# Kernel optimization log

Measured on AMD Instinct MI355X. Metric: run time of the kernel, lower is better.

Reference implementation:

```python
import jax, jax.numpy as jnp
import numpy as np
from jax.ops import segment_sum, segment_max

N = 100000          # nodes
E = 1600000         # edges
F_NODE = 128
F_EDGE = 32
HID = 64
ACT = 32
NG = 1000           # graph rows in y (repeat_factor = N // NG = 100)
NEG_SLOPE = 0.2


def _add_self_loops(src, dst, ea, n):
    # PyG add_self_loops with fill_value='mean': self-loop attr = mean of
    # incoming edge_attr per target node (0 for isolated nodes).
    cnt = segment_sum(jnp.ones((ea.shape[0],), ea.dtype), dst, num_segments=n)
    loop_attr = segment_sum(ea, dst, num_segments=n) / jnp.clip(cnt, 1.0)[:, None]
    ar = jnp.arange(n, dtype=src.dtype)
    return (jnp.concatenate([src, ar]),
            jnp.concatenate([dst, ar]),
            jnp.concatenate([ea, loop_attr], axis=0))


def _gatv2(xx, src, dst, ea, Wl, bl, Wr, br, We, att, bias, n):
    xl = xx @ Wl + bl                      # source transform  [n, HID]
    xr = xx @ Wr + br                      # target transform  [n, HID]
    e = ea @ We                            # edge embedding    [E', HID]
    m = jax.nn.leaky_relu(xl[src] + xr[dst] + e, NEG_SLOPE)
    logits = m @ att                       # [E']
    mx = segment_max(logits, dst, num_segments=n)
    ex = jnp.exp(logits - mx[dst])
    den = segment_sum(ex, dst, num_segments=n)
    alpha = ex / den[dst]                  # segment softmax over incoming edges
    return segment_sum(xl[src] * alpha[:, None], dst, num_segments=n) + bias


def setup_inputs() -> dict:
    key = jax.random.key(0)
    ks = jax.random.split(key, 32)
    g = lambda k, s: jax.random.normal(k, s, jnp.float32)
    p = lambda k, s: jax.random.normal(k, s, jnp.float32) * 0.05
    return {
        "x": g(ks[0], (N, F_NODE)),
        "edge_attr": g(ks[1], (E, F_EDGE)),
        "y": g(ks[2], (2 * NG,)),
        "Wl1": p(ks[3], (F_NODE, HID)), "bl1": p(ks[4], (HID,)),
        "Wr1": p(ks[5], (F_NODE, HID)), "br1": p(ks[6], (HID,)),
        "We1": p(ks[7], (F_EDGE, HID)), "att1": p(ks[8], (HID,)),
        "bias1": p(ks[9], (HID,)),
        "Wl2": p(ks[10], (HID, HID)), "bl2": p(ks[11], (HID,)),
        "Wr2": p(ks[12], (HID, HID)), "br2": p(ks[13], (HID,)),
        "We2": p(ks[14], (F_EDGE, HID)), "att2": p(ks[15], (HID,)),
        "bias2": p(ks[16], (HID,)),
        "W0": p(ks[17], (2, 2)), "b0": p(ks[18], (2,)),
        "W1": p(ks[19], (HID + 2, 32)), "b1": p(ks[20], (32,)),
        "W2": p(ks[21], (32, ACT)), "b2": p(ks[22], (ACT,)),
        "edge_index": jax.random.randint(ks[23], (2, E), 0, N),
        "node_idx": jax.random.randint(ks[24], (1000,), 0, N),
    }


def reference(x, edge_attr, y, Wl1, bl1, Wr1, br1, We1, att1, bias1,
              Wl2, bl2, Wr2, br2, We2, att2, bias2,
              W0, b0, W1, b1, W2, b2, edge_index, node_idx):
    n = x.shape[0]
    src, dst, ea = _add_self_loops(edge_index[0], edge_index[1], edge_attr, n)
    h = jax.nn.relu(_gatv2(x, src, dst, ea, Wl1, bl1, Wr1, br1, We1, att1, bias1, n))
    h = jax.nn.relu(_gatv2(h, src, dst, ea, Wl2, bl2, Wr2, br2, We2, att2, bias2, n))
    yr = y.reshape(-1, 2)
    repeat_factor = n // yr.shape[0]
    yr = jnp.repeat(yr, repeat_factor, axis=0)          # [n, 2]
    yr = jax.nn.relu(yr @ W0 + b0)
    z = jnp.concatenate([h, yr], axis=1)                # [n, HID+2]
    z = jax.nn.relu(z @ W1 + b1)
    z = z @ W2 + b2                                     # [n, ACT]
    return z[node_idx]
```

## Files before the change

kernel.cpp:

```cpp
#include <hip/hip_runtime.h>


#define NF1CAP 24576

__device__ __forceinline__ int getbit(const unsigned* b, int i) {
    return (b[i >> 5] >> (i & 31)) & 1;
}

__global__ __launch_bounds__(256)
void mark_sel_kernel(const int* __restrict__ nidx, unsigned* __restrict__ selbits,
                     unsigned* __restrict__ f1bits, int n)
{
    int t = blockIdx.x * blockDim.x + threadIdx.x;
    if (t < n) {
        int i = nidx[t];
        atomicOr(&selbits[i >> 5], 1u << (i & 31));
        atomicOr(&f1bits[i >> 5], 1u << (i & 31));
    }
}

__global__ __launch_bounds__(256)
void pass_a_kernel(const int* __restrict__ src, const int* __restrict__ dst,
                   const unsigned* __restrict__ selbits,
                   unsigned* __restrict__ f1bits, int* __restrict__ indeg, int E)
{
    int E4 = E >> 2;
    for (int i = blockIdx.x * blockDim.x + threadIdx.x; i < E4;
         i += gridDim.x * blockDim.x) {
        int4 d4 = ((const int4*)dst)[i];
        int dd[4] = {d4.x, d4.y, d4.z, d4.w};
#pragma unroll
        for (int j = 0; j < 4; ++j) {
            int d = dd[j];
            atomicAdd(&indeg[d], 1);
            if (getbit(selbits, d)) {
                int s = src[i * 4 + j];
                atomicOr(&f1bits[s >> 5], 1u << (s & 31));
            }
        }
    }
    int t = blockIdx.x * blockDim.x + threadIdx.x;
    if (t < (E & 3)) {
        int e = (E4 << 2) + t;
        int d = dst[e];
        atomicAdd(&indeg[d], 1);
        if (getbit(selbits, d)) {
            int s = src[e];
            atomicOr(&f1bits[s >> 5], 1u << (s & 31));
        }
    }
}

__global__ __launch_bounds__(256)
void compact_f1_kernel(const unsigned* __restrict__ f1bits, int* __restrict__ nf1,
                       int* __restrict__ f1node, int* __restrict__ slot_of, int n)
{
    int i = blockIdx.x * blockDim.x + threadIdx.x;
    if (i >= n) return;
    if (getbit(f1bits, i)) {
        int s = atomicAdd(nf1, 1);
        if (s < NF1CAP) { f1node[s] = i; slot_of[i] = s; }
        else slot_of[i] = 0;
    }
}

__global__ __launch_bounds__(1024)
void scan_kernel(const int* __restrict__ indeg, const int* __restrict__ f1node,
                 const int* __restrict__ n_ptr, int cap,
                 int* __restrict__ offs, int* __restrict__ ne_out)
{
    __shared__ int buf[1024];
    int n = *n_ptr; if (n > cap) n = cap;
    int tid = threadIdx.x;
    int chunk = (n + 1023) / 1024;
    int base = tid * chunk;
    int s = 0;
    for (int j = 0; j < chunk; ++j) {
        int idx = base + j;
        if (idx < n) s += indeg[f1node[idx]];
    }
    buf[tid] = s;
    __syncthreads();
    for (int off = 1; off < 1024; off <<= 1) {
        int v = (tid >= off) ? buf[tid - off] : 0;
        __syncthreads();
        buf[tid] += v;
        __syncthreads();
    }
    int run = (tid > 0) ? buf[tid - 1] : 0;
    for (int j = 0; j < chunk; ++j) {
        int idx = base + j;
        if (idx < n) { offs[idx] = run; run += indeg[f1node[idx]]; }
    }
    if (tid == 1023) { offs[n] = buf[1023]; *ne_out = buf[1023]; }
}

__global__ __launch_bounds__(256)
void scatter_kernel(const int* __restrict__ src, const int* __restrict__ dst,
                    const unsigned* __restrict__ f1bits,
                    const int* __restrict__ slot_of, const int* __restrict__ aoffs,
                    int* __restrict__ cursor,
                    unsigned long long* __restrict__ apack, int E)
{
    int E4 = E >> 2;
    for (int i = blockIdx.x * blockDim.x + threadIdx.x; i < E4;
         i += gridDim.x * blockDim.x) {
        int4 d4 = ((const int4*)dst)[i];
        int dd[4] = {d4.x, d4.y, d4.z, d4.w};
#pragma unroll
        for (int j = 0; j < 4; ++j) {
            int d = dd[j];
            if (!getbit(f1bits, d)) continue;
            int a = slot_of[d];
            int pos = aoffs[a] + atomicAdd(&cursor[a], 1);
            int e = i * 4 + j;
            apack[pos] = (unsigned long long)(unsigned)e
                       | ((unsigned long long)(unsigned)src[e] << 21)
                       | ((unsigned long long)(unsigned)a << 38);
        }
    }
    int t = blockIdx.x * blockDim.x + threadIdx.x;
    if (t < (E & 3)) {
        int e = (E4 << 2) + t;
        int d = dst[e];
        if (getbit(f1bits, d)) {
            int a = slot_of[d];
            int pos = aoffs[a] + atomicAdd(&cursor[a], 1);
            apack[pos] = (unsigned long long)(unsigned)e
                       | ((unsigned long long)(unsigned)src[e] << 21)
                       | ((unsigned long long)(unsigned)a << 38);
        }
    }
}

__global__ __launch_bounds__(256)
void gemm1_fused_kernel(const float* __restrict__ X,
                        const float* __restrict__ Wl, const float* __restrict__ bl,
                        const float* __restrict__ Wr, const float* __restrict__ br,
                        const int* __restrict__ f1node,
                        const int* __restrict__ nf1_p,
                        int ndense, int gb_dense,
                        float* __restrict__ outl, float* __restrict__ outr)
{
    constexpr int K = 128, BM = 128, BK = 32, LDA = BM + 4;
    __shared__ float sW[K * 64];
    __shared__ float sA[BK * LDA];
    bool dense = (int)blockIdx.x < gb_dense;
    const float* W = dense ? Wl : Wr;
    const float* bias = dense ? bl : br;
    const int* rowlist = dense ? nullptr : f1node;
    float* out = dense ? outl : outr;
    int rows;
    if (dense) rows = ndense;
    else { rows = *nf1_p; if (rows > NF1CAP) rows = NF1CAP; }
    int bid = dense ? (int)blockIdx.x : (int)blockIdx.x - gb_dense;
    int base = bid * BM;
    if (base >= rows) return;
    int tid = threadIdx.x;
    for (int t = tid; t < K * 16; t += 256)
        ((float4*)sW)[t] = ((const float4*)W)[t];
    int tx = tid & 7, ty = tid >> 3;
    int c0 = tx * 8;
    float acc[4][8];
#pragma unroll
    for (int i = 0; i < 4; ++i)
#pragma unroll
        for (int j = 0; j < 8; ++j) acc[i][j] = 0.f;

    for (int kb = 0; kb < K; kb += BK) {
        __syncthreads();
#pragma unroll
        for (int q = 0; q < 4; ++q) {
            int lin = q * 256 + tid;
            int m = lin >> 3;
            int kk = (lin & 7) * 4;
            int rr = base + m;
            if (rr >= rows) rr = rows - 1;
            int grow = rowlist ? rowlist[rr] : rr;
            float4 v = *(const float4*)&X[(size_t)grow * K + kb + kk];
            sA[(kk + 0) * LDA + m] = v.x;
            sA[(kk + 1) * LDA + m] = v.y;
            sA[(kk + 2) * LDA + m] = v.z;
            sA[(kk + 3) * LDA + m] = v.w;
        }
        __syncthreads();
#pragma unroll
        for (int k = 0; k < BK; ++k) {
            float4 a4 = *(const float4*)&sA[k * LDA + ty * 4];
            float4 w0 = *(const float4*)&sW[(kb + k) * 64 + c0];
            float4 w1 = *(const float4*)&sW[(kb + k) * 64 + c0 + 4];
            float av[4] = {a4.x, a4.y, a4.z, a4.w};
            float wv[8] = {w0.x, w0.y, w0.z, w0.w, w1.x, w1.y, w1.z, w1.w};
#pragma unroll
            for (int i = 0; i < 4; ++i)
#pragma unroll
                for (int j = 0; j < 8; ++j)
                    acc[i][j] += av[i] * wv[j];
        }
    }
    float bv[8];
#pragma unroll
    for (int j = 0; j < 8; ++j) bv[j] = bias[c0 + j];
#pragma unroll
    for (int i = 0; i < 4; ++i) {
        int r = base + ty * 4 + i;
        if (r < rows) {
            float o[8];
#pragma unroll
            for (int j = 0; j < 8; ++j) o[j] = acc[i][j] + bv[j];
            *(float4*)&out[(size_t)r * 64 + c0] = *(float4*)&o[0];
            *(float4*)&out[(size_t)r * 64 + c0 + 4] = *(float4*)&o[4];
        }
    }
}

__global__ __launch_bounds__(256)
void gemm2_both_kernel(const float* __restrict__ X,
                       const float* __restrict__ Wl, const float* __restrict__ bl,
                       const float* __restrict__ Wr, const float* __restrict__ br,
                       const int* __restrict__ nf1_p,
                       float* __restrict__ outl, float* __restrict__ outr)
{
    constexpr int K = 64, BM = 128, BK = 32, LDA = BM + 4;
    __shared__ float sW[2 * K * 64];
    __shared__ float sA[BK * LDA];
    int rows = *nf1_p; if (rows > NF1CAP) rows = NF1CAP;
    int base = (int)blockIdx.x * BM;
    if (base >= rows) return;
    int tid = threadIdx.x;
    for (int t = tid; t < K * 16; t += 256) {
        ((float4*)sW)[t] = ((const float4*)Wl)[t];
        ((float4*)sW)[K * 16 + t] = ((const float4*)Wr)[t];
    }
    int tx = tid & 7, ty = tid >> 3;
    int c0 = tx * 8;
    float accl[4][8], accr[4][8];
#pragma unroll
    for (int i = 0; i < 4; ++i)
#pragma unroll
        for (int j = 0; j < 8; ++j) { accl[i][j] = 0.f; accr[i][j] = 0.f; }

    for (int kb = 0; kb < K; kb += BK) {
        __syncthreads();
#pragma unroll
        for (int q = 0; q < 4; ++q) {
            int lin = q * 256 + tid;
            int m = lin >> 3;
            int kk = (lin & 7) * 4;
            int rr = base + m;
            if (rr >= rows) rr = rows - 1;
            float4 v = *(const float4*)&X[(size_t)rr * K + kb + kk];
            sA[(kk + 0) * LDA + m] = v.x;
            sA[(kk + 1) * LDA + m] = v.y;
            sA[(kk + 2) * LDA + m] = v.z;
            sA[(kk + 3) * LDA + m] = v.w;
        }
        __syncthreads();
#pragma unroll
        for (int k = 0; k < BK; ++k) {
            float4 a4 = *(const float4*)&sA[k * LDA + ty * 4];
            float4 l0 = *(const float4*)&sW[(kb + k) * 64 + c0];
            float4 l1 = *(const float4*)&sW[(kb + k) * 64 + c0 + 4];
            float4 r0 = *(const float4*)&sW[K * 64 + (kb + k) * 64 + c0];
            float4 r1 = *(const float4*)&sW[K * 64 + (kb + k) * 64 + c0 + 4];
            float av[4] = {a4.x, a4.y, a4.z, a4.w};
            float lv[8] = {l0.x, l0.y, l0.z, l0.w, l1.x, l1.y, l1.z, l1.w};
            float rv[8] = {r0.x, r0.y, r0.z, r0.w, r1.x, r1.y, r1.z, r1.w};
#pragma unroll
            for (int i = 0; i < 4; ++i)
#pragma unroll
                for (int j = 0; j < 8; ++j) {
                    accl[i][j] += av[i] * lv[j];
                    accr[i][j] += av[i] * rv[j];
                }
        }
    }
    float blv[8], brv[8];
#pragma unroll
    for (int j = 0; j < 8; ++j) { blv[j] = bl[c0 + j]; brv[j] = br[c0 + j]; }
#pragma unroll
    for (int i = 0; i < 4; ++i) {
        int r = base + ty * 4 + i;
        if (r < rows) {
            float ol[8], orr[8];
#pragma unroll
            for (int j = 0; j < 8; ++j) {
                ol[j] = accl[i][j] + blv[j];
                orr[j] = accr[i][j] + brv[j];
            }
            *(float4*)&outl[(size_t)r * 64 + c0] = *(float4*)&ol[0];
            *(float4*)&outl[(size_t)r * 64 + c0 + 4] = *(float4*)&ol[4];
            *(float4*)&outr[(size_t)r * 64 + c0] = *(float4*)&orr[0];
            *(float4*)&outr[(size_t)r * 64 + c0 + 4] = *(float4*)&orr[4];
        }
    }
}

__global__ __launch_bounds__(256)
void agg1_kernel(const int* __restrict__ nf1_p, const int* __restrict__ f1node,
                 const int* __restrict__ aoffs,
                 const unsigned long long* __restrict__ apack,
                 const float* __restrict__ eattr,
                 const float* __restrict__ xl, const float* __restrict__ xrc,
                 const float* __restrict__ We, const float* __restrict__ att,
                 const float* __restrict__ bias, float* __restrict__ h1c)
{
    constexpr int LDE = 36;
    __shared__ float sAttr[64 * LDE];
    __shared__ int   sSrc[64];
    __shared__ int   sEid[64];
    __shared__ float sLog[64];
    __shared__ float sRedM[4], sRedD[4];
    __shared__ float sCol[8][32];
    __shared__ float sMean[32];
    __shared__ float sAcc[4][64];

    int tid = threadIdx.x, lane = tid & 63, w = tid >> 6;
    float wec[32];
#pragma unroll
    for (int k = 0; k < 32; ++k) wec[k] = We[k * 64 + lane];
    float att_l = att[lane], bias_l = bias[lane];
    int n = *nf1_p; if (n > NF1CAP) n = NF1CAP;

    for (int a = blockIdx.x; a < n; a += gridDim.x) {
        int i = f1node[a];
        int beg = aoffs[a], deg = aoffs[a + 1] - beg;
        float xl_i = xl[(size_t)i * 64 + lane];
        float xr_i = xrc[(size_t)a * 64 + lane];
        float run_m = -3.0e38f, run_den = 0.f, accw = 0.f, colsum = 0.f;

        for (int t0 = 0; t0 < deg; t0 += 64) {
            int tn = deg - t0; if (tn > 64) tn = 64;
            __syncthreads();
            if (tid < tn) {
                unsigned long long rec = apack[beg + t0 + tid];
                sEid[tid] = (int)(rec & 0x1FFFFF);
                sSrc[tid] = (int)((rec >> 21) & 0x1FFFF);
            }
            __syncthreads();
#pragma unroll
            for (int q = 0; q < 2; ++q) {
                int lin = q * 256 + tid;
                int el = lin >> 3, quad = lin & 7;
                if (el < tn) {
                    float4 v = ((const float4*)(eattr
                                 + (size_t)sEid[el] * 32))[quad];
                    *(float4*)&sAttr[el * LDE + quad * 4] = v;
                }
            }
            __syncthreads();
            for (int r = tid >> 5; r < tn; r += 8)
                colsum += sAttr[r * LDE + (tid & 31)];
            for (int j = w; j < tn; j += 4) {
                const float* ar = &sAttr[j * LDE];
                float emb = 0.f;
#pragma unroll
                for (int k = 0; k < 32; ++k) emb += ar[k] * wec[k];
                float m = xl[(size_t)sSrc[j] * 64 + lane] + xr_i + emb;
                m = (m >= 0.f) ? m : 0.2f * m;
                float pf = m * att_l;
#pragma unroll
                for (int d = 32; d; d >>= 1) pf += __shfl_xor(pf, d, 64);
                if (lane == 0) sLog[j] = pf;
            }
            __syncthreads();
            float wm = (tid < tn) ? sLog[tid] : -3.0e38f;
#pragma unroll
            for (int d = 32; d; d >>= 1) wm = fmaxf(wm, __shfl_xor(wm, d, 64));
            if (lane == 0) sRedM[w] = wm;
            __syncthreads();
            float bm = fmaxf(fmaxf(sRedM[0], sRedM[1]),
                             fmaxf(sRedM[2], sRedM[3]));
            float newm = fmaxf(run_m, bm);
            float dp = (tid < tn) ? __expf(sLog[tid] - newm) : 0.f;
#pragma unroll
            for (int d = 32; d; d >>= 1) dp += __shfl_xor(dp, d, 64);
            if (lane == 0) sRedD[w] = dp;
            __syncthreads();
            float bden = sRedD[0] + sRedD[1] + sRedD[2] + sRedD[3];
            float sc = __expf(run_m - newm);
            accw *= sc;
            run_den = run_den * sc + bden;
            int j = w;
            for (; j + 8 <= tn + w; j += 8) {
                int j1 = j + 4;
                float w0 = __expf(sLog[j] - newm);
                float v0 = xl[(size_t)sSrc[j] * 64 + lane];
                float w1 = (j1 < tn) ? __expf(sLog[j1] - newm) : 0.f;
                float v1 = (j1 < tn) ? xl[(size_t)sSrc[j1] * 64 + lane] : 0.f;
                accw += w0 * v0;
                accw += w1 * v1;
            }
            for (; j < tn; j += 4) {
                float wgt = __expf(sLog[j] - newm);
                accw += wgt * xl[(size_t)sSrc[j] * 64 + lane];
            }
            run_m = newm;
        }
        sCol[tid >> 5][tid & 31] = colsum;
        __syncthreads();
        if (tid < 32) {
            float s = 0.f;
#pragma unroll
            for (int r = 0; r < 8; ++r) s += sCol[r][tid];
            sMean[tid] = s / (float)(deg > 0 ? deg : 1);
        }
        __syncthreads();
        float embs = 0.f;
#pragma unroll
        for (int k = 0; k < 32; ++k) embs += sMean[k] * wec[k];
        float ms = xl_i + xr_i + embs;
        ms = (ms >= 0.f) ? ms : 0.2f * ms;
        float pf = ms * att_l;
#pragma unroll
        for (int d = 32; d; d >>= 1) pf += __shfl_xor(pf, d, 64);
        float slog = pf;
        float newm = fmaxf(run_m, slog);
        float sc = __expf(run_m - newm);
        float wself = __expf(slog - newm);
        float den = run_den * sc + wself;
        sAcc[w][lane] = accw * sc;
        __syncthreads();
        float tot = sAcc[0][lane] + sAcc[1][lane] + sAcc[2][lane]
                  + sAcc[3][lane] + wself * xl_i;
        h1c[(size_t)a * 64 + lane] = fmaxf(tot / den + bias_l, 0.f);
        __syncthreads();
    }
}

__global__ __launch_bounds__(256)
void tail2_kernel(const int* __restrict__ nidx, const int* __restrict__ slot_of,
                  const int* __restrict__ aoffs,
                  const unsigned long long* __restrict__ apack,
                  const float* __restrict__ eattr,
                  const float* __restrict__ xl2c, const float* __restrict__ xr2c,
                  const float* __restrict__ We, const float* __restrict__ att,
                  const float* __restrict__ bias, const float* __restrict__ y,
                  const float* __restrict__ W0, const float* __restrict__ b0,
                  const float* __restrict__ W1, const float* __restrict__ b1,
                  const float* __restrict__ W2, const float* __restrict__ b2,
                  float* __restrict__ out, int nsel, int rf)
{
    constexpr int LDE = 36;
    __shared__ float sAttr[64 * LDE];
    __shared__ int   sSrc[64];
    __shared__ int   sEid[64];
    __shared__ float sLog[64];
    __shared__ float sRedM[4], sRedD[4];
    __shared__ float sCol[8][32];
    __shared__ float sMean[32];
    __shared__ float sAcc[4][64];

    int tid = threadIdx.x, lane = tid & 63, w = tid >> 6;
    float wec[32];
#pragma unroll
    for (int k = 0; k < 32; ++k) wec[k] = We[k * 64 + lane];
    float att_l = att[lane], bias_l = bias[lane];

    for (int r = blockIdx.x; r < nsel; r += gridDim.x) {
        int i = nidx[r];
        int a = slot_of[i];
        int beg = aoffs[a], deg = aoffs[a + 1] - beg;
        float xl_i = xl2c[(size_t)a * 64 + lane];
        float xr_i = xr2c[(size_t)a * 64 + lane];
        float run_m = -3.0e38f, run_den = 0.f, accw = 0.f, colsum = 0.f;

        for (int t0 = 0; t0 < deg; t0 += 64) {
            int tn = deg - t0; if (tn > 64) tn = 64;
            __syncthreads();
            if (tid < tn) {
                unsigned long long rec = apack[beg + t0 + tid];
                sEid[tid] = (int)(rec & 0x1FFFFF);
                sSrc[tid] = slot_of[(int)((rec >> 21) & 0x1FFFF)];
            }
            __syncthreads();
#pragma unroll
            for (int q = 0; q < 2; ++q) {
                int lin = q * 256 + tid;
                int el = lin >> 3, quad = lin & 7;
                if (el < tn) {
                    float4 v = ((const float4*)(eattr
                                 + (size_t)sEid[el] * 32))[quad];
                    *(float4*)&sAttr[el * LDE + quad * 4] = v;
                }
            }
            __syncthreads();
            for (int rr = tid >> 5; rr < tn; rr += 8)
                colsum += sAttr[rr * LDE + (tid & 31)];
            for (int j = w; j < tn; j += 4) {
                const float* ar = &sAttr[j * LDE];
                float emb = 0.f;
#pragma unroll
                for (int k = 0; k < 32; ++k) emb += ar[k] * wec[k];
                float m = xl2c[(size_t)sSrc[j] * 64 + lane] + xr_i + emb;
                m = (m >= 0.f) ? m : 0.2f * m;
                float pf = m * att_l;
#pragma unroll
                for (int d = 32; d; d >>= 1) pf += __shfl_xor(pf, d, 64);
                if (lane == 0) sLog[j] = pf;
            }
            __syncthreads();
            float wm = (tid < tn) ? sLog[tid] : -3.0e38f;
#pragma unroll
            for (int d = 32; d; d >>= 1) wm = fmaxf(wm, __shfl_xor(wm, d, 64));
            if (lane == 0) sRedM[w] = wm;
            __syncthreads();
            float bm = fmaxf(fmaxf(sRedM[0], sRedM[1]),
                             fmaxf(sRedM[2], sRedM[3]));
            float newm = fmaxf(run_m, bm);
            float dp = (tid < tn) ? __expf(sLog[tid] - newm) : 0.f;
#pragma unroll
            for (int d = 32; d; d >>= 1) dp += __shfl_xor(dp, d, 64);
            if (lane == 0) sRedD[w] = dp;
            __syncthreads();
            float bden = sRedD[0] + sRedD[1] + sRedD[2] + sRedD[3];
            float sc = __expf(run_m - newm);
            accw *= sc;
            run_den = run_den * sc + bden;
            for (int j = w; j < tn; j += 4) {
                float wgt = __expf(sLog[j] - newm);
                accw += wgt * xl2c[(size_t)sSrc[j] * 64 + lane];
            }
            run_m = newm;
        }
        sCol[tid >> 5][tid & 31] = colsum;
        __syncthreads();
        if (tid < 32) {
            float s = 0.f;
#pragma unroll
            for (int rr = 0; rr < 8; ++rr) s += sCol[rr][tid];
            sMean[tid] = s / (float)(deg > 0 ? deg : 1);
        }
        __syncthreads();
        float embs = 0.f;
#pragma unroll
        for (int k = 0; k < 32; ++k) embs += sMean[k] * wec[k];
        float ms = xl_i + xr_i + embs;
        ms = (ms >= 0.f) ? ms : 0.2f * ms;
        float pf = ms * att_l;
#pragma unroll
        for (int d = 32; d; d >>= 1) pf += __shfl_xor(pf, d, 64);
        float slog = pf;
        float newm = fmaxf(run_m, slog);
        float sc = __expf(run_m - newm);
        float wself = __expf(slog - newm);
        float den = run_den * sc + wself;
        sAcc[w][lane] = accw * sc;
        __syncthreads();
        float tot = sAcc[0][lane] + sAcc[1][lane] + sAcc[2][lane]
                  + sAcc[3][lane] + wself * xl_i;
        float h = fmaxf(tot / den + bias_l, 0.f);
        int yi = i / rf;
        float y0 = y[2 * yi], y1 = y[2 * yi + 1];
        float t0v = fmaxf(y0 * W0[0] + y1 * W0[2] + b0[0], 0.f);
        float t1v = fmaxf(y0 * W0[1] + y1 * W0[3] + b0[1], 0.f);
        int j = lane & 31;
        float acc = b1[j];
#pragma unroll
        for (int k = 0; k < 64; ++k) acc += __shfl(h, k, 64) * W1[k * 32 + j];
        acc += t0v * W1[64 * 32 + j] + t1v * W1[65 * 32 + j];
        acc = fmaxf(acc, 0.f);
        float res = b2[j];
#pragma unroll
        for (int k = 0; k < 32; ++k) res += __shfl(acc, k, 64) * W2[k * 32 + j];
        if (w == 0 && lane < 32) out[(size_t)r * 32 + j] = res;
        __syncthreads();
    }
}

extern "C" void kernel_launch(void* const* d_in, const int* in_sizes, int n_in,
                              void* d_out, int out_size, void* d_ws,
                              size_t ws_size, hipStream_t stream)
{
    const float* x     = (const float*)d_in[0];
    const float* eattr = (const float*)d_in[1];
    const float* y     = (const float*)d_in[2];
    const float* Wl1 = (const float*)d_in[3],  *bl1 = (const float*)d_in[4];
    const float* Wr1 = (const float*)d_in[5],  *br1 = (const float*)d_in[6];
    const float* We1 = (const float*)d_in[7],  *att1 = (const float*)d_in[8];
    const float* bias1 = (const float*)d_in[9];
    const float* Wl2 = (const float*)d_in[10], *bl2 = (const float*)d_in[11];
    const float* Wr2 = (const float*)d_in[12], *br2 = (const float*)d_in[13];
    const float* We2 = (const float*)d_in[14], *att2 = (const float*)d_in[15];
    const float* bias2 = (const float*)d_in[16];
    const float* W0 = (const float*)d_in[17], *b0 = (const float*)d_in[18];
    const float* W1 = (const float*)d_in[19], *b1 = (const float*)d_in[20];
    const float* W2 = (const float*)d_in[21], *b2 = (const float*)d_in[22];
    const int* eidx = (const int*)d_in[23];
    const int* nidx = (const int*)d_in[24];

    const int N = in_sizes[0] / 128;
    const int E = in_sizes[1] / 32;
    const int NSEL = in_sizes[24];
    const int NGr = in_sizes[2] / 2;
    const int rf = N / NGr;

    const int* src = eidx;
    const int* dst = eidx + E;

    size_t off = 0;
    auto alloc = [&](size_t nb) {
        size_t r = off;
        off += (nb + 255) & ~(size_t)255;
        return r;
    };
    char* ws = (char*)d_ws;
    const int NBW = (N + 31) / 32;

    unsigned* selbits = (unsigned*)(ws + alloc((size_t)NBW * 4));
    unsigned* f1bits  = (unsigned*)(ws + alloc((size_t)NBW * 4));
    int* indeg  = (int*)(ws + alloc((size_t)N * 4));
    int* cursor = (int*)(ws + alloc((size_t)NF1CAP * 4));
    int* ctrs   = (int*)(ws + alloc(256));
    size_t zero_bytes = off;
    int* slot_of = (int*)(ws + alloc((size_t)N * 4));
    int* f1node  = (int*)(ws + alloc((size_t)NF1CAP * 4));
    int* aoffs   = (int*)(ws + alloc((size_t)(NF1CAP + 1) * 4));
    unsigned long long* apack =
        (unsigned long long*)(ws + alloc((size_t)E * 8));
    float* xl1  = (float*)(ws + alloc((size_t)N * 64 * 4));
    float* xr1c = (float*)(ws + alloc((size_t)NF1CAP * 64 * 4));
    float* h1c  = (float*)(ws + alloc((size_t)NF1CAP * 64 * 4));
    float* xl2c = (float*)(ws + alloc((size_t)NF1CAP * 64 * 4));
    float* xr2c = (float*)(ws + alloc((size_t)NF1CAP * 64 * 4));
    (void)ws_size;

    int* nf1_p = ctrs + 0;
    int* ne1_p = ctrs + 1;

    hipMemsetAsync(ws, 0, zero_bytes, stream);

    mark_sel_kernel<<<(NSEL + 255) / 256, 256, 0, stream>>>(nidx, selbits,
                                                            f1bits, NSEL);
    pass_a_kernel<<<2048, 256, 0, stream>>>(src, dst, selbits, f1bits, indeg, E);
    compact_f1_kernel<<<(N + 255) / 256, 256, 0, stream>>>(f1bits, nf1_p,
                                                           f1node, slot_of, N);
    scan_kernel<<<1, 1024, 0, stream>>>(indeg, f1node, nf1_p, NF1CAP, aoffs,
                                        ne1_p);
    scatter_kernel<<<2048, 256, 0, stream>>>(src, dst, f1bits, slot_of, aoffs,
                                             cursor, apack, E);
    {
        int gb_dense = (N + 127) / 128;
        int gb_total = gb_dense + NF1CAP / 128;
        gemm1_fused_kernel<<<gb_total, 256, 0, stream>>>(
            x, Wl1, bl1, Wr1, br1, f1node, nf1_p, N, gb_dense, xl1, xr1c);
    }
    agg1_kernel<<<4096, 256, 0, stream>>>(nf1_p, f1node, aoffs, apack, eattr,
                                          xl1, xr1c, We1, att1, bias1, h1c);
    gemm2_both_kernel<<<NF1CAP / 128, 256, 0, stream>>>(h1c, Wl2, bl2, Wr2,
                                                        br2, nf1_p, xl2c, xr2c);
    tail2_kernel<<<NSEL, 256, 0, stream>>>(nidx, slot_of, aoffs, apack, eattr,
                                           xl2c, xr2c, We2, att2, bias2, y,
                                           W0, b0, W1, b1, W2, b2,
                                           (float*)d_out, NSEL, rf);
}
```

Measured before the change: 670.5 us.

## Map one wavefront per node in GAT aggregation and filter degree histogram

Both aggregation kernels now give each 64-lane wavefront its own destination node instead of a 256-thread block. Each wave stages 16 edges at a time in private shared memory and uses an online softmax per edge, which removes the block-level __syncthreads and cross-wave reductions. The self-loop mean embedding is now the mean of the per-edge embeddings, using linearity, instead of a column sum of attributes. The edge pass is split in two so in-degree atomics only hit nodes in the needed frontier, at the cost of a second read of dst. The per-edge serial online softmax adds exp work and a dependency chain per edge.

```diff
diff --git a/kernel.cpp b/kernel.cpp
--- a/kernel.cpp
+++ b/kernel.cpp
@@ -20,9 +20,9 @@
 }
 
 __global__ __launch_bounds__(256)
-void pass_a_kernel(const int* __restrict__ src, const int* __restrict__ dst,
-                   const unsigned* __restrict__ selbits,
-                   unsigned* __restrict__ f1bits, int* __restrict__ indeg, int E)
+void pass_mark_kernel(const int* __restrict__ src, const int* __restrict__ dst,
+                      const unsigned* __restrict__ selbits,
+                      unsigned* __restrict__ f1bits, int E)
 {
     int E4 = E >> 2;
     for (int i = blockIdx.x * blockDim.x + threadIdx.x; i < E4;
@@ -31,23 +31,41 @@
         int dd[4] = {d4.x, d4.y, d4.z, d4.w};
 #pragma unroll
         for (int j = 0; j < 4; ++j) {
-            int d = dd[j];
-            atomicAdd(&indeg[d], 1);
-            if (getbit(selbits, d)) {
+            if (getbit(selbits, dd[j])) {
                 int s = src[i * 4 + j];
                 atomicOr(&f1bits[s >> 5], 1u << (s & 31));
             }
         }
+    }
+    int t = blockIdx.x * blockDim.x + threadIdx.x;
+    if (t < (E & 3)) {
+        int e = (E4 << 2) + t;
+        if (getbit(selbits, dst[e])) {
+            int s = src[e];
+            atomicOr(&f1bits[s >> 5], 1u << (s & 31));
+        }
+    }
+}
+
+__global__ __launch_bounds__(256)
+void pass_hist_kernel(const int* __restrict__ dst,
+                      const unsigned* __restrict__ f1bits,
+                      int* __restrict__ indeg, int E)
+{
+    int E4 = E >> 2;
+    for (int i = blockIdx.x * blockDim.x + threadIdx.x; i < E4;
+         i += gridDim.x * blockDim.x) {
+        int4 d4 = ((const int4*)dst)[i];
+        int dd[4] = {d4.x, d4.y, d4.z, d4.w};
+#pragma unroll
+        for (int j = 0; j < 4; ++j)
+            if (getbit(f1bits, dd[j])) atomicAdd(&indeg[dd[j]], 1);
     }
     int t = blockIdx.x * blockDim.x + threadIdx.x;
     if (t < (E & 3)) {
         int e = (E4 << 2) + t;
         int d = dst[e];
-        atomicAdd(&indeg[d], 1);
-        if (getbit(selbits, d)) {
-            int s = src[e];
-            atomicOr(&f1bits[s >> 5], 1u << (s & 31));
-        }
+        if (getbit(f1bits, d)) atomicAdd(&indeg[d], 1);
     }
 }
 
@@ -305,126 +323,74 @@
                  const float* __restrict__ We, const float* __restrict__ att,
                  const float* __restrict__ bias, float* __restrict__ h1c)
 {
-    constexpr int LDE = 36;
-    __shared__ float sAttr[64 * LDE];
-    __shared__ int   sSrc[64];
-    __shared__ int   sEid[64];
-    __shared__ float sLog[64];
-    __shared__ float sRedM[4], sRedD[4];
-    __shared__ float sCol[8][32];
-    __shared__ float sMean[32];
-    __shared__ float sAcc[4][64];
-
+    __shared__ float sAttr[4 * 16 * 36];
     int tid = threadIdx.x, lane = tid & 63, w = tid >> 6;
+    float* myAttr = &sAttr[w * 16 * 36];
     float wec[32];
 #pragma unroll
     for (int k = 0; k < 32; ++k) wec[k] = We[k * 64 + lane];
     float att_l = att[lane], bias_l = bias[lane];
     int n = *nf1_p; if (n > NF1CAP) n = NF1CAP;
-
-    for (int a = blockIdx.x; a < n; a += gridDim.x) {
+    int gwid = (blockIdx.x * 256 + tid) >> 6;
+    int nwaves = (gridDim.x * 256) >> 6;
+
+    for (int a = gwid; a < n; a += nwaves) {
         int i = f1node[a];
         int beg = aoffs[a], deg = aoffs[a + 1] - beg;
         float xl_i = xl[(size_t)i * 64 + lane];
         float xr_i = xrc[(size_t)a * 64 + lane];
-        float run_m = -3.0e38f, run_den = 0.f, accw = 0.f, colsum = 0.f;
-
-        for (int t0 = 0; t0 < deg; t0 += 64) {
-            int tn = deg - t0; if (tn > 64) tn = 64;
-            __syncthreads();
-            if (tid < tn) {
-                unsigned long long rec = apack[beg + t0 + tid];
-                sEid[tid] = (int)(rec & 0x1FFFFF);
-                sSrc[tid] = (int)((rec >> 21) & 0x1FFFF);
+        float run_m = -3.0e38f, run_den = 0.f, accw = 0.f, embsum = 0.f;
+
+        for (int t0 = 0; t0 < deg; t0 += 16) {
+            int rem = deg - t0; if (rem > 16) rem = 16;
+            unsigned long long rec = 0;
+            if (lane < rem) rec = apack[beg + t0 + lane];
+            int eidv = (int)(rec & 0x1FFFFF);
+            int srcv = (int)((rec >> 21) & 0x1FFFF);
+            asm volatile("" ::: "memory");
+#pragma unroll
+            for (int q = 0; q < 2; ++q) {
+                int row = (lane >> 3) + q * 8;
+                int quad = lane & 7;
+                int rowc = (row < rem) ? row : rem - 1;
+                int e = __shfl(eidv, rowc, 64);
+                float4 v = ((const float4*)(eattr + (size_t)e * 32))[quad];
+                *(float4*)&myAttr[row * 36 + quad * 4] = v;
             }
-            __syncthreads();
-#pragma unroll
-            for (int q = 0; q < 2; ++q) {
-                int lin = q * 256 + tid;
-                int el = lin >> 3, quad = lin & 7;
-                if (el < tn) {
-                    float4 v = ((const float4*)(eattr
-                                 + (size_t)sEid[el] * 32))[quad];
-                    *(float4*)&sAttr[el * LDE + quad * 4] = v;
-                }
-            }
-            __syncthreads();
-            for (int r = tid >> 5; r < tn; r += 8)
-                colsum += sAttr[r * LDE + (tid & 31)];
-            for (int j = w; j < tn; j += 4) {
-                const float* ar = &sAttr[j * LDE];
+            asm volatile("" ::: "memory");
+            for (int j = 0; j < rem; ++j) {
+                const float* ar = &myAttr[j * 36];
                 float emb = 0.f;
 #pragma unroll
                 for (int k = 0; k < 32; ++k) emb += ar[k] * wec[k];
-                float m = xl[(size_t)sSrc[j] * 64 + lane] + xr_i + emb;
+                embsum += emb;
+                int s = __shfl(srcv, j, 64);
+                float xls = xl[(size_t)s * 64 + lane];
+                float m = xls + xr_i + emb;
                 m = (m >= 0.f) ? m : 0.2f * m;
                 float pf = m * att_l;
 #pragma unroll
                 for (int d = 32; d; d >>= 1) pf += __shfl_xor(pf, d, 64);
-                if (lane == 0) sLog[j] = pf;
+                float newm = fmaxf(run_m, pf);
+                float sc = __expf(run_m - newm);
+                float wgt = __expf(pf - newm);
+                accw = accw * sc + wgt * xls;
+                run_den = run_den * sc + wgt;
+                run_m = newm;
             }
-            __syncthreads();
-            float wm = (tid < tn) ? sLog[tid] : -3.0e38f;
-#pragma unroll
-            for (int d = 32; d; d >>= 1) wm = fmaxf(wm, __shfl_xor(wm, d, 64));
-            if (lane == 0) sRedM[w] = wm;
-            __syncthreads();
-            float bm = fmaxf(fmaxf(sRedM[0], sRedM[1]),
-                             fmaxf(sRedM[2], sRedM[3]));
-            float newm = fmaxf(run_m, bm);
-            float dp = (tid < tn) ? __expf(sLog[tid] - newm) : 0.f;
-#pragma unroll
-            for (int d = 32; d; d >>= 1) dp += __shfl_xor(dp, d, 64);
-            if (lane == 0) sRedD[w] = dp;
-            __syncthreads();
-            float bden = sRedD[0] + sRedD[1] + sRedD[2] + sRedD[3];
-            float sc = __expf(run_m - newm);
-            accw *= sc;
-            run_den = run_den * sc + bden;
-            int j = w;
-            for (; j + 8 <= tn + w; j += 8) {
-                int j1 = j + 4;
-                float w0 = __expf(sLog[j] - newm);
-                float v0 = xl[(size_t)sSrc[j] * 64 + lane];
-                float w1 = (j1 < tn) ? __expf(sLog[j1] - newm) : 0.f;
-                float v1 = (j1 < tn) ? xl[(size_t)sSrc[j1] * 64 + lane] : 0.f;
-                accw += w0 * v0;
-                accw += w1 * v1;
-            }
-            for (; j < tn; j += 4) {
-                float wgt = __expf(sLog[j] - newm);
-                accw += wgt * xl[(size_t)sSrc[j] * 64 + lane];
-            }
-            run_m = newm;
-        }
-        sCol[tid >> 5][tid & 31] = colsum;
-        __syncthreads();
-        if (tid < 32) {
-            float s = 0.f;
-#pragma unroll
-            for (int r = 0; r < 8; ++r) s += sCol[r][tid];
-            sMean[tid] = s / (float)(deg > 0 ? deg : 1);
-        }
-        __syncthreads();
-        float embs = 0.f;
-#pragma unroll
-        for (int k = 0; k < 32; ++k) embs += sMean[k] * wec[k];
-        float ms = xl_i + xr_i + embs;
+        }
+        float inv = 1.0f / (float)(deg > 0 ? deg : 1);
+        float ms = xl_i + xr_i + embsum * inv;
         ms = (ms >= 0.f) ? ms : 0.2f * ms;
         float pf = ms * att_l;
 #pragma unroll
         for (int d = 32; d; d >>= 1) pf += __shfl_xor(pf, d, 64);
-        float slog = pf;
-        float newm = fmaxf(run_m, slog);
+        float newm = fmaxf(run_m, pf);
         float sc = __expf(run_m - newm);
-        float wself = __expf(slog - newm);
+        float wself = __expf(pf - newm);
+        accw = accw * sc + wself * xl_i;
         float den = run_den * sc + wself;
-        sAcc[w][lane] = accw * sc;
-        __syncthreads();
-        float tot = sAcc[0][lane] + sAcc[1][lane] + sAcc[2][lane]
-                  + sAcc[3][lane] + wself * xl_i;
-        h1c[(size_t)a * 64 + lane] = fmaxf(tot / den + bias_l, 0.f);
-        __syncthreads();
+        h1c[(size_t)a * 64 + lane] = fmaxf(accw / den + bias_l, 0.f);
     }
 }
 
@@ -441,115 +407,75 @@
                   const float* __restrict__ W2, const float* __restrict__ b2,
                   float* __restrict__ out, int nsel, int rf)
 {
-    constexpr int LDE = 36;
-    __shared__ float sAttr[64 * LDE];
-    __shared__ int   sSrc[64];
-    __shared__ int   sEid[64];
-    __shared__ float sLog[64];
-    __shared__ float sRedM[4], sRedD[4];
-    __shared__ float sCol[8][32];
-    __shared__ float sMean[32];
-    __shared__ float sAcc[4][64];
-
+    __shared__ float sAttr[4 * 16 * 36];
     int tid = threadIdx.x, lane = tid & 63, w = tid >> 6;
+    float* myAttr = &sAttr[w * 16 * 36];
     float wec[32];
 #pragma unroll
     for (int k = 0; k < 32; ++k) wec[k] = We[k * 64 + lane];
     float att_l = att[lane], bias_l = bias[lane];
-
-    for (int r = blockIdx.x; r < nsel; r += gridDim.x) {
+    int gwid = (blockIdx.x * 256 + tid) >> 6;
+    int nwaves = (gridDim.x * 256) >> 6;
+
+    for (int r = gwid; r < nsel; r += nwaves) {
         int i = nidx[r];
         int a = slot_of[i];
         int beg = aoffs[a], deg = aoffs[a + 1] - beg;
         float xl_i = xl2c[(size_t)a * 64 + lane];
         float xr_i = xr2c[(size_t)a * 64 + lane];
-        float run_m = -3.0e38f, run_den = 0.f, accw = 0.f, colsum = 0.f;
-
-        for (int t0 = 0; t0 < deg; t0 += 64) {
-            int tn = deg - t0; if (tn > 64) tn = 64;
-            __syncthreads();
-            if (tid < tn) {
-                unsigned long long rec = apack[beg + t0 + tid];
-                sEid[tid] = (int)(rec & 0x1FFFFF);
-                sSrc[tid] = slot_of[(int)((rec >> 21) & 0x1FFFF)];
+        float run_m = -3.0e38f, run_den = 0.f, accw = 0.f, embsum = 0.f;
+
+        for (int t0 = 0; t0 < deg; t0 += 16) {
+            int rem = deg - t0; if (rem > 16) rem = 16;
+            unsigned long long rec = 0;
+            if (lane < rem) rec = apack[beg + t0 + lane];
+            int eidv = (int)(rec & 0x1FFFFF);
+            int srcv = (int)((rec >> 21) & 0x1FFFF);
+            asm volatile("" ::: "memory");
+#pragma unroll
+            for (int q = 0; q < 2; ++q) {
+                int row = (lane >> 3) + q * 8;
+                int quad = lane & 7;
+                int rowc = (row < rem) ? row : rem - 1;
+                int e = __shfl(eidv, rowc, 64);
+                float4 v = ((const float4*)(eattr + (size_t)e * 32))[quad];
+                *(float4*)&myAttr[row * 36 + quad * 4] = v;
             }
-            __syncthreads();
-#pragma unroll
-            for (int q = 0; q < 2; ++q) {
-                int lin = q * 256 + tid;
-                int el = lin >> 3, quad = lin & 7;
-                if (el < tn) {
-                    float4 v = ((const float4*)(eattr
-                                 + (size_t)sEid[el] * 32))[quad];
-                    *(float4*)&sAttr[el * LDE + quad * 4] = v;
-                }
-            }
-            __syncthreads();
-            for (int rr = tid >> 5; rr < tn; rr += 8)
-                colsum += sAttr[rr * LDE + (tid & 31)];
-            for (int j = w; j < tn; j += 4) {
-                const float* ar = &sAttr[j * LDE];
+            asm volatile("" ::: "memory");
+            for (int j = 0; j < rem; ++j) {
+                const float* ar = &myAttr[j * 36];
                 float emb = 0.f;
 #pragma unroll
                 for (int k = 0; k < 32; ++k) emb += ar[k] * wec[k];
-                float m = xl2c[(size_t)sSrc[j] * 64 + lane] + xr_i + emb;
+                embsum += emb;
+                int s = __shfl(srcv, j, 64);
+                int sslot = slot_of[s];
+                float xls = xl2c[(size_t)sslot * 64 + lane];
+                float m = xls + xr_i + emb;
                 m = (m >= 0.f) ? m : 0.2f * m;
                 float pf = m * att_l;
 #pragma unroll
                 for (int d = 32; d; d >>= 1) pf += __shfl_xor(pf, d, 64);
-                if (lane == 0) sLog[j] = pf;
+                float newm = fmaxf(run_m, pf);
+                float sc = __expf(run_m - newm);
+                float wgt = __expf(pf - newm);
+                accw = accw * sc + wgt * xls;
+                run_den = run_den * sc + wgt;
+                run_m = newm;
             }
-            __syncthreads();
-            float wm = (tid < tn) ? sLog[tid] : -3.0e38f;
-#pragma unroll
-            for (int d = 32; d; d >>= 1) wm = fmaxf(wm, __shfl_xor(wm, d, 64));
-            if (lane == 0) sRedM[w] = wm;
-            __syncthreads();
-            float bm = fmaxf(fmaxf(sRedM[0], sRedM[1]),
-                             fmaxf(sRedM[2], sRedM[3]));
-            float newm = fmaxf(run_m, bm);
-            float dp = (tid < tn) ? __expf(sLog[tid] - newm) : 0.f;
-#pragma unroll
-            for (int d = 32; d; d >>= 1) dp += __shfl_xor(dp, d, 64);
-            if (lane == 0) sRedD[w] = dp;
-            __syncthreads();
-            float bden = sRedD[0] + sRedD[1] + sRedD[2] + sRedD[3];
-            float sc = __expf(run_m - newm);
-            accw *= sc;
-            run_den = run_den * sc + bden;
-            for (int j = w; j < tn; j += 4) {
-                float wgt = __expf(sLog[j] - newm);
-                accw += wgt * xl2c[(size_t)sSrc[j] * 64 + lane];
-            }
-            run_m = newm;
-        }
-        sCol[tid >> 5][tid & 31] = colsum;
-        __syncthreads();
-        if (tid < 32) {
-            float s = 0.f;
-#pragma unroll
-            for (int rr = 0; rr < 8; ++rr) s += sCol[rr][tid];
-            sMean[tid] = s / (float)(deg > 0 ? deg : 1);
-        }
-        __syncthreads();
-        float embs = 0.f;
-#pragma unroll
-        for (int k = 0; k < 32; ++k) embs += sMean[k] * wec[k];
-        float ms = xl_i + xr_i + embs;
+        }
+        float inv = 1.0f / (float)(deg > 0 ? deg : 1);
+        float ms = xl_i + xr_i + embsum * inv;
         ms = (ms >= 0.f) ? ms : 0.2f * ms;
         float pf = ms * att_l;
 #pragma unroll
         for (int d = 32; d; d >>= 1) pf += __shfl_xor(pf, d, 64);
-        float slog = pf;
-        float newm = fmaxf(run_m, slog);
+        float newm = fmaxf(run_m, pf);
         float sc = __expf(run_m - newm);
-        float wself = __expf(slog - newm);
+        float wself = __expf(pf - newm);
+        accw = accw * sc + wself * xl_i;
         float den = run_den * sc + wself;
-        sAcc[w][lane] = accw * sc;
-        __syncthreads();
-        float tot = sAcc[0][lane] + sAcc[1][lane] + sAcc[2][lane]
-                  + sAcc[3][lane] + wself * xl_i;
-        float h = fmaxf(tot / den + bias_l, 0.f);
+        float h = fmaxf(accw / den + bias_l, 0.f);
         int yi = i / rf;
         float y0 = y[2 * yi], y1 = y[2 * yi + 1];
         float t0v = fmaxf(y0 * W0[0] + y1 * W0[2] + b0[0], 0.f);
@@ -563,8 +489,7 @@
         float res = b2[j];
 #pragma unroll
         for (int k = 0; k < 32; ++k) res += __shfl(acc, k, 64) * W2[k * 32 + j];
-        if (w == 0 && lane < 32) out[(size_t)r * 32 + j] = res;
-        __syncthreads();
+        if (lane < 32) out[(size_t)r * 32 + j] = res;
     }
 }
 
@@ -632,7 +557,8 @@
 
     mark_sel_kernel<<<(NSEL + 255) / 256, 256, 0, stream>>>(nidx, selbits,
                                                             f1bits, NSEL);
-    pass_a_kernel<<<2048, 256, 0, stream>>>(src, dst, selbits, f1bits, indeg, E);
+    pass_mark_kernel<<<2048, 256, 0, stream>>>(src, dst, selbits, f1bits, E);
+    pass_hist_kernel<<<2048, 256, 0, stream>>>(dst, f1bits, indeg, E);
     compact_f1_kernel<<<(N + 255) / 256, 256, 0, stream>>>(f1bits, nf1_p,
                                                            f1node, slot_of, N);
     scan_kernel<<<1, 1024, 0, stream>>>(indeg, f1node, nf1_p, NF1CAP, aoffs,
@@ -645,12 +571,11 @@
         gemm1_fused_kernel<<<gb_total, 256, 0, stream>>>(
             x, Wl1, bl1, Wr1, br1, f1node, nf1_p, N, gb_dense, xl1, xr1c);
     }
-    agg1_kernel<<<4096, 256, 0, stream>>>(nf1_p, f1node, aoffs, apack, eattr,
+    agg1_kernel<<<1024, 256, 0, stream>>>(nf1_p, f1node, aoffs, apack, eattr,
                                           xl1, xr1c, We1, att1, bias1, h1c);
     gemm2_both_kernel<<<NF1CAP / 128, 256, 0, stream>>>(h1c, Wl2, bl2, Wr2,
                                                         br2, nf1_p, xl2c, xr2c);
-    tail2_kernel<<<NSEL, 256, 0, stream>>>(nidx, slot_of, aoffs, apack, eattr,
-                                           xl2c, xr2c, We2, att2, bias2, y,
-                                           W0, b0, W1, b1, W2, b2,
-                                           (float*)d_out, NSEL, rf);
-}
+    tail2_kernel<<<(NSEL + 3) / 4, 256, 0, stream>>>(
+        nidx, slot_of, aoffs, apack, eattr, xl2c, xr2c, We2, att2, bias2, y,
+        W0, b0, W1, b1, W2, b2, (float*)d_out, NSEL, rf);
+}
```

New measurement: 569.6 us. 15.1% less time.
